# Kernel tuning notes

Measured on AMD Instinct MI355X. Metric: run time of the kernel, lower is better.

The kernel has to match this reference:

```python
import jax, jax.numpy as jnp
import numpy as np

B, N, E = 4, 20000, 320000
DA, DB, H, OUT = 64, 64, 128, 1  # feature dims, hidden_dim, output_dim; DA+DB == H


def setup_inputs() -> dict:
    key = jax.random.key(0)
    ks = jax.random.split(key, 9)
    feat_a = jax.random.normal(ks[0], (B, N, DA), dtype=jnp.float32)
    feat_b = jax.random.normal(ks[1], (B, N, DB), dtype=jnp.float32)
    edge_index = jax.random.randint(ks[2], (2, E), 0, N)
    s = 1.0 / np.sqrt(H)
    W_gcn = jax.random.normal(ks[3], (H, H), dtype=jnp.float32) * s
    b_gcn = jnp.zeros((H,), dtype=jnp.float32)
    W1 = jax.random.normal(ks[4], (H, H), dtype=jnp.float32) * s
    b1 = jax.random.normal(ks[5], (H,), dtype=jnp.float32) * 0.01
    W2 = jax.random.normal(ks[6], (H, OUT), dtype=jnp.float32) * s
    b2 = jnp.zeros((OUT,), dtype=jnp.float32)
    return {"feat_a": feat_a, "feat_b": feat_b, "edge_index": edge_index,
            "W_gcn": W_gcn, "b_gcn": b_gcn, "W1": W1, "b1": b1, "W2": W2, "b2": b2}


def _gcn_conv(x, src, dst, W, b):
    # x: [B, N, H_in]; GCNConv: out = D^-1/2 (A+I) D^-1/2 (x W) + b
    n = x.shape[1]
    loops = jnp.arange(n)
    src_sl = jnp.concatenate([src, loops])  # add self-loops
    dst_sl = jnp.concatenate([dst, loops])
    deg = jax.ops.segment_sum(jnp.ones_like(src_sl, dtype=x.dtype), dst_sl, num_segments=n)
    dinv = jnp.where(deg > 0, jax.lax.rsqrt(deg), 0.0)
    norm = dinv[src_sl] * dinv[dst_sl]  # [E+N]
    h = x @ W  # [B, N, H]

    def agg(hb):  # hb: [N, H]
        msgs = hb[src_sl] * norm[:, None]  # gather + scale, [E+N, H]
        return jax.ops.segment_sum(msgs, dst_sl, num_segments=n)  # scatter-add

    return jax.vmap(agg)(h) + b


def reference(feat_a, feat_b, edge_index, W_gcn, b_gcn, W1, b1, W2, b2):
    combined = jnp.concatenate([feat_a, feat_b], axis=-1)  # [B, N, H]
    gcn_out = _gcn_conv(combined, edge_index[0], edge_index[1], W_gcn, b_gcn)
    pooled = gcn_out.mean(axis=1)  # mean over nodes -> [B, H]
    hid = jax.nn.relu(pooled @ W1 + b1)  # dropout is identity in eval
    logits = hid @ W2 + b2  # [B, 1]
    return logits
```

## Files before the change

kernel.cpp:

```cpp
#include <hip/hip_runtime.h>

#define NB 4
#define NN 20000
#define NE 320000
#define HH 128

#define EBLK 64
#define HTHR 1024
#define CHUNKS 256
#define WTHR 512
#define PER 79
#define TOTW CHUNKS
#define NSEC 8

#define RB 79

#define OFF_PDEG 0
#define OFF_DINV (EBLK * NN)
#define OFF_PS   (OFF_DINV + NN)
#define OFF_V    (OFF_PS + EBLK * NN)
#define OFF_CNT  (OFF_V + NSEC * NB * HH)

__global__ void __launch_bounds__(HTHR) deg_hist_kernel(
        const int* __restrict__ dst, float* __restrict__ pdeg) {
    __shared__ float hist[NN];
    const int t = threadIdx.x, bk = blockIdx.x;
    for (int i = t; i < NN; i += HTHR) hist[i] = 0.0f;
    __syncthreads();
    for (int e = bk * HTHR + t; e < NE; e += EBLK * HTHR)
        atomicAdd(&hist[dst[e]], 1.0f);
    __syncthreads();
    float* out = pdeg + (size_t)bk * NN;
    for (int i = t; i < NN; i += HTHR) out[i] = hist[i];
}

__global__ void reduce_deg_kernel(const float* __restrict__ pdeg,
                                  float* __restrict__ dinv,
                                  float* __restrict__ v, int* __restrict__ counter) {
    if (blockIdx.x == 0) {
        #pragma unroll
        for (int u = 0; u < NSEC * NB * HH / 256; ++u)
            v[u * 256 + threadIdx.x] = 0.0f;
        if (threadIdx.x == 0) *counter = 0;
    }
    const int n = blockIdx.x * 256 + threadIdx.x;
    if (n >= NN) return;
    float acc = 1.0f;
    #pragma unroll 8
    for (int c = 0; c < EBLK; ++c) acc += pdeg[(size_t)c * NN + n];
    dinv[n] = rsqrtf(acc);
}

__global__ void __launch_bounds__(HTHR) s_hist_kernel(
        const int* __restrict__ src, const int* __restrict__ dst,
        const float* __restrict__ dinv, float* __restrict__ ps) {
    __shared__ float hist[NN];
    const int t = threadIdx.x, bk = blockIdx.x;
    for (int i = t; i < NN; i += HTHR) hist[i] = 0.0f;
    __syncthreads();
    for (int e = bk * HTHR + t; e < NE; e += EBLK * HTHR)
        atomicAdd(&hist[src[e]], dinv[dst[e]]);
    __syncthreads();
    float* out = ps + (size_t)bk * NN;
    for (int i = t; i < NN; i += HTHR) out[i] = hist[i];
}

__global__ void __launch_bounds__(WTHR) wsum_mlp_kernel(
        const float* __restrict__ fa, const float* __restrict__ fb,
        const float* __restrict__ dinv, const float* __restrict__ ps,
        const float* __restrict__ Wg, const float* __restrict__ bg,
        const float* __restrict__ W1, const float* __restrict__ b1,
        const float* __restrict__ W2, const float* __restrict__ b2,
        float* __restrict__ v, int* __restrict__ counter,
        float* __restrict__ out) {
    __shared__ float wl[PER];
    __shared__ float wpart[PER][8];
    __shared__ float4 smem[WTHR];
    __shared__ int lastflag;
    const int t = threadIdx.x;
    const int c = blockIdx.x;
    const int n0 = c * PER;
    const int n1 = min(NN, n0 + PER);
    const int cnt = n1 - n0;
    float* vsec = v + (size_t)(c & (NSEC - 1)) * (NB * HH);

    if (cnt > 0) {
        for (int idx = t; idx < cnt * 8; idx += WTHR) {
            const int i = idx >> 3, s = idx & 7;
            const int n = n0 + i;
            float a = 0.0f;
            #pragma unroll
            for (int u = 0; u < 8; ++u) a += ps[(size_t)(s * 8 + u) * NN + n];
            wpart[i][s] = a;
        }
        __syncthreads();
        for (int i = t; i < cnt; i += WTHR) {
            float a = 0.0f;
            #pragma unroll
            for (int s = 0; s < 8; ++s) a += wpart[i][s];
            const float di = dinv[n0 + i];
            wl[i] = di * (di + a);
        }
        __syncthreads();

        const int g = t >> 5;
        const int q = t & 31;
        const float* base = (q < 16) ? (fa + (size_t)q * 4)
                                     : (fb + (size_t)(q - 16) * 4);

        float4 acc[NB];
        #pragma unroll
        for (int b = 0; b < NB; ++b) acc[b] = make_float4(0.f, 0.f, 0.f, 0.f);

        int n = n0 + g;
        for (; n + 48 < n1; n += 64) {
            const float w0 = wl[n - n0];
            const float w1 = wl[n + 16 - n0];
            const float w2 = wl[n + 32 - n0];
            const float w3 = wl[n + 48 - n0];
            #pragma unroll
            for (int b = 0; b < NB; ++b) {
                const float* p = base + ((size_t)b * NN + n) * 64;
                float4 x0 = *reinterpret_cast<const float4*>(p);
                float4 x1 = *reinterpret_cast<const float4*>(p + 16 * 64);
                float4 x2 = *reinterpret_cast<const float4*>(p + 32 * 64);
                float4 x3 = *reinterpret_cast<const float4*>(p + 48 * 64);
                acc[b].x += w0 * x0.x + w1 * x1.x + w2 * x2.x + w3 * x3.x;
                acc[b].y += w0 * x0.y + w1 * x1.y + w2 * x2.y + w3 * x3.y;
                acc[b].z += w0 * x0.z + w1 * x1.z + w2 * x2.z + w3 * x3.z;
                acc[b].w += w0 * x0.w + w1 * x1.w + w2 * x2.w + w3 * x3.w;
            }
        }
        for (; n < n1; n += 16) {
            const float wn = wl[n - n0];
            #pragma unroll
            for (int b = 0; b < NB; ++b) {
                float4 x = *reinterpret_cast<const float4*>(
                    base + ((size_t)b * NN + n) * 64);
                acc[b].x += wn * x.x; acc[b].y += wn * x.y;
                acc[b].z += wn * x.z; acc[b].w += wn * x.w;
            }
        }

        #pragma unroll
        for (int b = 0; b < NB; ++b) {
            smem[t] = acc[b];
            __syncthreads();
            if (t < 32) {
                float4 r = smem[t];
                #pragma unroll
                for (int gg = 1; gg < 16; ++gg) {
                    float4 o = smem[gg * 32 + t];
                    r.x += o.x; r.y += o.y; r.z += o.z; r.w += o.w;
                }
                const int k = (t < 16) ? t * 4 : 64 + (t - 16) * 4;
                float* vb = vsec + b * HH + k;
                atomicAdd(vb + 0, r.x);
                atomicAdd(vb + 1, r.y);
                atomicAdd(vb + 2, r.z);
                atomicAdd(vb + 3, r.w);
            }
            __syncthreads();
        }
    }

    if (t == 0) {
        asm volatile("s_waitcnt vmcnt(0)" ::: "memory");
        int old = atomicAdd(counter, 1);
        lastflag = (old == TOTW - 1);
    }
    __syncthreads();
    if (!lastflag) return;

    __shared__ float xs[NB][HH];
    __shared__ float ys[NB][HH];
    __shared__ float red[NB][HH];
    const int bb = t >> 7;
    const int kk = t & (HH - 1);

    float val = 0.0f;
    #pragma unroll
    for (int s = 0; s < NSEC; ++s)
        val += atomicAdd(&v[s * (NB * HH) + t], 0.0f);
    xs[bb][kk] = val * (1.0f / NN);
    __syncthreads();

    float a1 = bg[kk];
    #pragma unroll 8
    for (int j = 0; j < HH; ++j) a1 += xs[bb][j] * Wg[j * HH + kk];
    ys[bb][kk] = a1;
    __syncthreads();

    float a2 = b1[kk];
    #pragma unroll 8
    for (int j = 0; j < HH; ++j) a2 += ys[bb][j] * W1[j * HH + kk];
    a2 = fmaxf(a2, 0.0f);
    red[bb][kk] = a2 * W2[kk];
    __syncthreads();

    #pragma unroll
    for (int off = HH / 2; off > 0; off >>= 1) {
        if (kk < off) red[bb][kk] += red[bb][kk + off];
        __syncthreads();
    }
    if (kk == 0) out[bb] = red[bb][0] + b2[0];
}

extern "C" void kernel_launch(void* const* d_in, const int* in_sizes, int n_in,
                              void* d_out, int out_size, void* d_ws, size_t ws_size,
                              hipStream_t stream) {
    const float* fa = (const float*)d_in[0];
    const float* fb = (const float*)d_in[1];
    const int*   ei = (const int*)d_in[2];
    const float* Wg = (const float*)d_in[3];
    const float* bg = (const float*)d_in[4];
    const float* W1 = (const float*)d_in[5];
    const float* b1 = (const float*)d_in[6];
    const float* W2 = (const float*)d_in[7];
    const float* b2 = (const float*)d_in[8];
    float* out = (float*)d_out;

    const int* src = ei;
    const int* dst = ei + NE;

    float* ws   = (float*)d_ws;
    float* pdeg = ws + OFF_PDEG;
    float* dinv = ws + OFF_DINV;
    float* ps   = ws + OFF_PS;
    float* v    = ws + OFF_V;
    int* counter = (int*)(ws + OFF_CNT);

    deg_hist_kernel<<<EBLK, HTHR, 0, stream>>>(dst, pdeg);

    reduce_deg_kernel<<<RB, 256, 0, stream>>>(pdeg, dinv, v, counter);

    s_hist_kernel<<<EBLK, HTHR, 0, stream>>>(src, dst, dinv, ps);

    wsum_mlp_kernel<<<CHUNKS, WTHR, 0, stream>>>(fa, fb, dinv, ps,
                                                 Wg, bg, W1, b1, W2, b2,
                                                 v, counter, out);
}
```

Baseline: 54.61 us.

## Use dedicated spinning block for MLP tail with hierarchical completion counters

Adds an extra block 0 that preloads W_gcn and warms W1 into LDS/cache, then spin-waits on a master counter until every chunk block has finished. It then runs the pooled-mean and MLP tail from shared memory. Completion counting is split into 8 sub-counters feeding one master counter, which reduces contention on a single atomic. The goal is to hide the weight loads behind the main reduction and shorten the serial tail, at the cost of a block that occupies a CU while spinning and about 64KB more LDS per block, which may lower occupancy for every block.

```diff
diff --git a/kernel.cpp b/kernel.cpp
--- a/kernel.cpp
+++ b/kernel.cpp
@@ -10,7 +10,6 @@
 #define CHUNKS 256
 #define WTHR 512
 #define PER 79
-#define TOTW CHUNKS
 #define NSEC 8
 
 #define RB 79
@@ -36,12 +35,12 @@
 
 __global__ void reduce_deg_kernel(const float* __restrict__ pdeg,
                                   float* __restrict__ dinv,
-                                  float* __restrict__ v, int* __restrict__ counter) {
+                                  float* __restrict__ v, int* __restrict__ cnts) {
     if (blockIdx.x == 0) {
         #pragma unroll
         for (int u = 0; u < NSEC * NB * HH / 256; ++u)
             v[u * 256 + threadIdx.x] = 0.0f;
-        if (threadIdx.x == 0) *counter = 0;
+        if (threadIdx.x < 9) cnts[threadIdx.x] = 0;
     }
     const int n = blockIdx.x * 256 + threadIdx.x;
     if (n >= NN) return;
@@ -71,14 +70,70 @@
         const float* __restrict__ Wg, const float* __restrict__ bg,
         const float* __restrict__ W1, const float* __restrict__ b1,
         const float* __restrict__ W2, const float* __restrict__ b2,
-        float* __restrict__ v, int* __restrict__ counter,
+        float* __restrict__ v, int* __restrict__ cnts,
         float* __restrict__ out) {
+    __shared__ float WL[HH * HH];
+    __shared__ float xs[NB * HH];
+    __shared__ float ys[NB * HH];
+    __shared__ float red[NB * HH];
     __shared__ float wl[PER];
     __shared__ float wpart[PER][8];
     __shared__ float4 smem[WTHR];
-    __shared__ int lastflag;
+    int* sub = cnts;
+    int* master = cnts + 8;
     const int t = threadIdx.x;
-    const int c = blockIdx.x;
+
+    if (blockIdx.x == 0) {
+        const float4* wgv = (const float4*)Wg;
+        const float4* w1v = (const float4*)W1;
+        float4* wlv = (float4*)WL;
+        float warm = 0.0f;
+        for (int i = t; i < HH * HH / 4; i += WTHR) {
+            wlv[i] = wgv[i];
+            float4 y = w1v[i];
+            warm += y.x + y.w;
+        }
+        asm volatile("" :: "v"(warm));
+        if (t == 0) {
+            while (atomicAdd(master, 0) < NSEC) __builtin_amdgcn_s_sleep(8);
+        }
+        __syncthreads();
+
+        float val = 0.0f;
+        #pragma unroll
+        for (int s = 0; s < NSEC; ++s)
+            val += atomicAdd(&v[s * (NB * HH) + t], 0.0f);
+        xs[t] = val * (1.0f / NN);
+        __syncthreads();
+
+        const int bb = t >> 7;
+        const int kk = t & (HH - 1);
+
+        float a1 = bg[kk];
+        #pragma unroll 8
+        for (int j = 0; j < HH; ++j) a1 += xs[bb * HH + j] * WL[j * HH + kk];
+        ys[t] = a1;
+        __syncthreads();
+
+        for (int i = t; i < HH * HH / 4; i += WTHR) wlv[i] = w1v[i];
+        __syncthreads();
+        float a2 = b1[kk];
+        #pragma unroll 8
+        for (int j = 0; j < HH; ++j) a2 += ys[bb * HH + j] * WL[j * HH + kk];
+        a2 = fmaxf(a2, 0.0f);
+        red[t] = a2 * W2[kk];
+        __syncthreads();
+
+        #pragma unroll
+        for (int off = HH / 2; off > 0; off >>= 1) {
+            if (kk < off) red[bb * HH + kk] += red[bb * HH + kk + off];
+            __syncthreads();
+        }
+        if (kk == 0) out[bb] = red[bb * HH] + b2[0];
+        return;
+    }
+
+    const int c = blockIdx.x - 1;
     const int n0 = c * PER;
     const int n1 = min(NN, n0 + PER);
     const int cnt = n1 - n0;
@@ -166,44 +221,9 @@
 
     if (t == 0) {
         asm volatile("s_waitcnt vmcnt(0)" ::: "memory");
-        int old = atomicAdd(counter, 1);
-        lastflag = (old == TOTW - 1);
-    }
-    __syncthreads();
-    if (!lastflag) return;
-
-    __shared__ float xs[NB][HH];
-    __shared__ float ys[NB][HH];
-    __shared__ float red[NB][HH];
-    const int bb = t >> 7;
-    const int kk = t & (HH - 1);
-
-    float val = 0.0f;
-    #pragma unroll
-    for (int s = 0; s < NSEC; ++s)
-        val += atomicAdd(&v[s * (NB * HH) + t], 0.0f);
-    xs[bb][kk] = val * (1.0f / NN);
-    __syncthreads();
-
-    float a1 = bg[kk];
-    #pragma unroll 8
-    for (int j = 0; j < HH; ++j) a1 += xs[bb][j] * Wg[j * HH + kk];
-    ys[bb][kk] = a1;
-    __syncthreads();
-
-    float a2 = b1[kk];
-    #pragma unroll 8
-    for (int j = 0; j < HH; ++j) a2 += ys[bb][j] * W1[j * HH + kk];
-    a2 = fmaxf(a2, 0.0f);
-    red[bb][kk] = a2 * W2[kk];
-    __syncthreads();
-
-    #pragma unroll
-    for (int off = HH / 2; off > 0; off >>= 1) {
-        if (kk < off) red[bb][kk] += red[bb][kk + off];
-        __syncthreads();
-    }
-    if (kk == 0) out[bb] = red[bb][0] + b2[0];
+        int old = atomicAdd(&sub[c & (NSEC - 1)], 1);
+        if (old == (CHUNKS / NSEC) - 1) atomicAdd(master, 1);
+    }
 }
 
 extern "C" void kernel_launch(void* const* d_in, const int* in_sizes, int n_in,
@@ -228,15 +248,15 @@
     float* dinv = ws + OFF_DINV;
     float* ps   = ws + OFF_PS;
     float* v    = ws + OFF_V;
-    int* counter = (int*)(ws + OFF_CNT);
+    int*   cnts = (int*)(ws + OFF_CNT);
 
     deg_hist_kernel<<<EBLK, HTHR, 0, stream>>>(dst, pdeg);
 
-    reduce_deg_kernel<<<RB, 256, 0, stream>>>(pdeg, dinv, v, counter);
+    reduce_deg_kernel<<<RB, 256, 0, stream>>>(pdeg, dinv, v, cnts);
 
     s_hist_kernel<<<EBLK, HTHR, 0, stream>>>(src, dst, dinv, ps);
 
-    wsum_mlp_kernel<<<CHUNKS, WTHR, 0, stream>>>(fa, fb, dinv, ps,
-                                                 Wg, bg, W1, b1, W2, b2,
-                                                 v, counter, out);
-}
+    wsum_mlp_kernel<<<CHUNKS + 1, WTHR, 0, stream>>>(fa, fb, dinv, ps,
+                                                     Wg, bg, W1, b1, W2, b2,
+                                                     v, cnts, out);
+}
```

Result: faster. 51.13 us (-6.4%).
